# Kernel tuning notes

Hardware: AMD Instinct MI355X
Metric: run time of the kernel (lower is better)

The kernel has to match this reference:

```python
import jax, jax.numpy as jnp
import numpy as np

N_NODES = 50000
N_EDGES = 800000
NFEAT, NHID, NCLASS = 512, 128, 64


def setup_inputs() -> dict:
    key = jax.random.key(0)
    ks = jax.random.split(key, 8)
    x = jax.random.normal(ks[0], (N_NODES, NFEAT), dtype=jnp.float32)
    # GraphConvolution params (uniform-ish init like reset_parameters, stdv = 1/sqrt(fan_out))
    W1 = jax.random.normal(ks[1], (NFEAT, NHID), dtype=jnp.float32) * (1.0 / np.sqrt(NHID))
    b1 = jnp.zeros((NHID,), dtype=jnp.float32)
    W2 = jax.random.normal(ks[2], (NHID, NCLASS), dtype=jnp.float32) * (1.0 / np.sqrt(NCLASS))
    b2 = jnp.zeros((NCLASS,), dtype=jnp.float32)
    # sparse normalized adjacency in COO form
    edge_row = jax.random.randint(ks[3], (N_EDGES,), 0, N_NODES, dtype=jnp.int32)
    edge_col = jax.random.randint(ks[4], (N_EDGES,), 0, N_NODES, dtype=jnp.int32)
    edge_val = jax.random.uniform(ks[5], (N_EDGES,), dtype=jnp.float32) * 0.1
    return {"x": x, "W1": W1, "b1": b1, "W2": W2, "b2": b2,
            "edge_val": edge_val, "edge_row": edge_row, "edge_col": edge_col}


def _spmm(feat, edge_row, edge_col, edge_val, n_nodes):
    # (adj @ feat) with adj given as COO: out[r] = sum_e val[e] * feat[c[e]]
    msg = feat[edge_col] * edge_val[:, None]          # [E, d]
    return jax.ops.segment_sum(msg, edge_row, num_segments=n_nodes)


def reference(x, W1, b1, W2, b2, edge_val, edge_row, edge_col):
    # eval mode: dropout = identity, use_bn = False
    n = x.shape[0]
    h = jax.nn.relu(_spmm(x @ W1, edge_row, edge_col, edge_val, n) + b1)  # gc1 + relu
    out = _spmm(h @ W2, edge_row, edge_col, edge_val, n) + b2             # gc2
    return out
```

## Files before the change

### kernel.cpp

```cpp
#include <hip/hip_runtime.h>

#define N_NODES 50000
#define N_EDGES 800000
#define NFEAT 512
#define NHID 128
#define NCLASS 64

#define SCAN_BLOCKS 49
#define ZERO_BLOCKS 49

using bf16x8 = __attribute__((ext_vector_type(8))) __bf16;
using f32x4  = __attribute__((ext_vector_type(4))) float;
using u16x8  = __attribute__((ext_vector_type(8))) unsigned short;
using u16x4  = __attribute__((ext_vector_type(4))) unsigned short;
typedef unsigned long long u64;

__device__ __forceinline__ unsigned short f2bf(float f)
{
    unsigned u = __builtin_bit_cast(unsigned, f);
    unsigned r = (u + 0x7FFFu + ((u >> 16) & 1u)) >> 16;
    return (unsigned short)r;
}
__device__ __forceinline__ float bf2f(unsigned short b)
{
    return __builtin_bit_cast(float, (unsigned)b << 16);
}
__device__ __forceinline__ u16x4 cvt4(float4 f)
{
    u16x4 h;
    h[0] = __builtin_bit_cast(unsigned short, (__bf16)f.x);
    h[1] = __builtin_bit_cast(unsigned short, (__bf16)f.y);
    h[2] = __builtin_bit_cast(unsigned short, (__bf16)f.z);
    h[3] = __builtin_bit_cast(unsigned short, (__bf16)f.w);
    return h;
}

__global__ void prep_kernel(int4* __restrict__ zp, int n4,
                            const float* __restrict__ W1, const float* __restrict__ W2,
                            unsigned short* __restrict__ W1t, unsigned short* __restrict__ W2t)
{
    const int b = blockIdx.x;
    if (b < ZERO_BLOCKS) {
        const int i = b * 256 + threadIdx.x;
        if (i < n4) zp[i] = make_int4(0, 0, 0, 0);
    } else {
        const int idx = (b - ZERO_BLOCKS) * 256 + threadIdx.x;
        if (idx < NFEAT * NHID) {
            const int n = idx / NFEAT, k = idx % NFEAT;
            W1t[idx] = f2bf(W1[k * NHID + n]);
        } else {
            const int j = idx - NFEAT * NHID;
            if (j < NHID * NCLASS) {
                const int n = j / NHID, k = j % NHID;
                W2t[j] = f2bf(W2[k * NCLASS + n]);
            }
        }
    }
}

__global__ __launch_bounds__(512) void gemm1_pipe(const float* __restrict__ A,
                                                  const unsigned short* __restrict__ Bt,
                                                  unsigned short* __restrict__ C, int M)
{
    constexpr int K = NFEAT, N = NHID, BM = 128, BK = 32, NSTEP = K / BK;
    constexpr int LDW = BK + 8;
    __shared__ unsigned short As[2][BM][LDW];
    __shared__ unsigned short Bs[2][N][LDW];

    const int tid  = threadIdx.x;
    const int wid  = tid >> 6;
    const int lane = tid & 63;
    const int lm   = lane & 15;
    const int lk   = (lane >> 4) * 8;
    const int m0   = blockIdx.x * BM;

    const int ar0 = tid >> 3;
    const int ac0 = (tid & 7) * 4;
    const int ga0 = (m0 + ar0      < M) ? (m0 + ar0)      : (M - 1);
    const int ga1 = (m0 + ar0 + 64 < M) ? (m0 + ar0 + 64) : (M - 1);
    const float* Arow0 = &A[(size_t)ga0 * K];
    const float* Arow1 = &A[(size_t)ga1 * K];
    const int bn = tid >> 2;
    const int bk = (tid & 3) * 8;
    const unsigned short* Brow = &Bt[(size_t)bn * K];

    f32x4 acc[8] = {};

    {
        float4 fa0 = *(const float4*)&Arow0[ac0];
        float4 fa1 = *(const float4*)&Arow1[ac0];
        u16x8  bv  = *(const u16x8*)&Brow[bk];
        *(u16x4*)&As[0][ar0][ac0]      = cvt4(fa0);
        *(u16x4*)&As[0][ar0 + 64][ac0] = cvt4(fa1);
        *(u16x8*)&Bs[0][bn][bk]        = bv;
    }
    __syncthreads();

    #pragma unroll
    for (int t = 0; t < NSTEP; ++t) {
        const int cur = t & 1;
        float4 na0, na1; u16x8 nb;
        if (t + 1 < NSTEP) {
            na0 = *(const float4*)&Arow0[(t + 1) * BK + ac0];
            na1 = *(const float4*)&Arow1[(t + 1) * BK + ac0];
            nb  = *(const u16x8*)&Brow[(t + 1) * BK + bk];
        }
        bf16x8 a = __builtin_bit_cast(bf16x8, *(const u16x8*)&As[cur][wid * 16 + lm][lk]);
        #pragma unroll
        for (int nf = 0; nf < 8; ++nf) {
            bf16x8 b = __builtin_bit_cast(bf16x8, *(const u16x8*)&Bs[cur][nf * 16 + lm][lk]);
            acc[nf] = __builtin_amdgcn_mfma_f32_16x16x32_bf16(a, b, acc[nf], 0, 0, 0);
        }
        if (t + 1 < NSTEP) {
            *(u16x4*)&As[cur ^ 1][ar0][ac0]      = cvt4(na0);
            *(u16x4*)&As[cur ^ 1][ar0 + 64][ac0] = cvt4(na1);
            *(u16x8*)&Bs[cur ^ 1][bn][bk]        = nb;
            __syncthreads();
        }
    }

    #pragma unroll
    for (int nf = 0; nf < 8; ++nf)
        #pragma unroll
        for (int r = 0; r < 4; ++r) {
            const int m = m0 + wid * 16 + (lane >> 4) * 4 + r;
            if (m < M) C[(size_t)m * N + nf * 16 + lm] =
                __builtin_bit_cast(unsigned short, (__bf16)acc[nf][r]);
        }
}

template<int K, int N>
__global__ __launch_bounds__(256) void gemm_mfma_bf16a(const unsigned short* __restrict__ A,
                                                       const unsigned short* __restrict__ Bt,
                                                       unsigned short* __restrict__ C, int M)
{
    constexpr int BM = 128, BK = 32, NF = N / 16;
    constexpr int LDW = BK + 8;
    __shared__ unsigned short As[BM][LDW];
    __shared__ unsigned short Bs[N][LDW];

    const int tid  = threadIdx.x;
    const int wid  = tid >> 6;
    const int lane = tid & 63;
    const int lm   = lane & 15;
    const int lk   = (lane >> 4) * 8;
    const int m0   = blockIdx.x * BM;

    f32x4 acc[2][NF] = {};

    for (int k0 = 0; k0 < K; k0 += BK) {
        if (k0) __syncthreads();
        {
            #pragma unroll
            for (int c = 0; c < 2; ++c) {
                const int chunk = tid * 2 + c;
                const int r  = chunk >> 2;
                const int kc = (chunk & 3) * 8;
                const int m  = m0 + r;
                u16x8 v = {};
                if (m < M) v = *(const u16x8*)&A[(size_t)m * K + k0 + kc];
                *(u16x8*)&As[r][kc] = v;
            }
        }
        {
            constexpr int CH  = (N * BK / 8) / 256;
            constexpr int CPR = BK / 8;
            #pragma unroll
            for (int c = 0; c < CH; ++c) {
                const int chunk = tid * CH + c;
                const int n  = chunk / CPR;
                const int kc = (chunk % CPR) * 8;
                *(u16x8*)&Bs[n][kc] = *(const u16x8*)&Bt[(size_t)n * K + k0 + kc];
            }
        }
        __syncthreads();

        bf16x8 a[2];
        #pragma unroll
        for (int mf = 0; mf < 2; ++mf)
            a[mf] = __builtin_bit_cast(bf16x8, *(const u16x8*)&As[wid * 32 + mf * 16 + lm][lk]);
        #pragma unroll
        for (int nf = 0; nf < NF; ++nf) {
            bf16x8 b = __builtin_bit_cast(bf16x8, *(const u16x8*)&Bs[nf * 16 + lm][lk]);
            #pragma unroll
            for (int mf = 0; mf < 2; ++mf)
                acc[mf][nf] = __builtin_amdgcn_mfma_f32_16x16x32_bf16(a[mf], b, acc[mf][nf], 0, 0, 0);
        }
    }

    #pragma unroll
    for (int mf = 0; mf < 2; ++mf)
        #pragma unroll
        for (int nf = 0; nf < NF; ++nf)
            #pragma unroll
            for (int r = 0; r < 4; ++r) {
                const int m = m0 + wid * 32 + mf * 16 + (lane >> 4) * 4 + r;
                if (m < M) C[(size_t)m * N + nf * 16 + lm] =
                    __builtin_bit_cast(unsigned short, (__bf16)acc[mf][nf][r]);
            }
}

__global__ void hist_rank_kernel(const int* __restrict__ er, int* __restrict__ counts,
                                 unsigned char* __restrict__ rank)
{
    int e = blockIdx.x * blockDim.x + threadIdx.x;
    if (e < N_EDGES) rank[e] = (unsigned char)atomicAdd(&counts[er[e]], 1);
}

__global__ __launch_bounds__(1024) void scan_blocks(const int* __restrict__ counts,
                                                    int* __restrict__ row_ptr,
                                                    int* __restrict__ bsums)
{
    __shared__ int tmp[1024];
    const int tid = threadIdx.x;
    const int gid = blockIdx.x * 1024 + tid;
    const int v = (gid < N_NODES) ? counts[gid] : 0;
    tmp[tid] = v;
    __syncthreads();
    #pragma unroll
    for (int off = 1; off < 1024; off <<= 1) {
        int t = (tid >= off) ? tmp[tid - off] : 0;
        __syncthreads();
        tmp[tid] += t;
        __syncthreads();
    }
    if (gid < N_NODES) row_ptr[gid] = tmp[tid] - v;
    if (tid == 1023) bsums[blockIdx.x] = tmp[1023];
}

__global__ __launch_bounds__(1024) void add_offsets2(int* __restrict__ row_ptr,
                                                     const int* __restrict__ bsums)
{
    __shared__ int soff;
    if (threadIdx.x < 64) {
        const int lane = threadIdx.x;
        const int orig = (lane < SCAN_BLOCKS) ? bsums[lane] : 0;
        int v = orig;
        #pragma unroll
        for (int off = 1; off < 64; off <<= 1) {
            int t = __shfl_up(v, off, 64);
            if (lane >= off) v += t;
        }
        if (lane == (int)blockIdx.x) soff = v - orig;
    }
    __syncthreads();
    const int gid = blockIdx.x * 1024 + threadIdx.x;
    if (gid < N_NODES) row_ptr[gid] += soff;
    if (gid == 0) row_ptr[N_NODES] = N_EDGES;
}

__global__ void scatter_cv(const int* __restrict__ er, const int* __restrict__ ec,
                           const float* __restrict__ ev, const unsigned char* __restrict__ rank,
                           const int* __restrict__ row_ptr, unsigned* __restrict__ cv)
{
    int e = blockIdx.x * blockDim.x + threadIdx.x;
    if (e >= N_EDGES) return;
    const int r = er[e];
    const int pos = row_ptr[r] + (int)rank[e];
    cv[pos] = ((unsigned)f2bf(ev[e]) << 16) | (unsigned)ec[e];
}

__global__ __launch_bounds__(256) void spmm_bf16_h(const unsigned short* __restrict__ feat,
                                                   const int* __restrict__ row_ptr,
                                                   const unsigned* __restrict__ cv,
                                                   const float* __restrict__ bias,
                                                   unsigned short* __restrict__ out)
{
    const int wave = blockIdx.x * (blockDim.x >> 6) + (threadIdx.x >> 6);
    const int lane = threadIdx.x & 63;
    if (wave >= N_NODES) return;
    const int beg = row_ptr[wave];
    const int end = row_ptr[wave + 1];
    const int deg = end - beg;
    const int n1 = deg < 64 ? deg : 64;

    unsigned pcv = 0;
    if (lane < n1) pcv = cv[beg + lane];
    const int half = lane >> 5;
    const int qi   = (lane & 31) * 4;

    float ax[4][4] = {};
    for (int u = 0; u < n1; u += 8) {
        unsigned p[4];
        #pragma unroll
        for (int g = 0; g < 4; ++g) {
            const int idx = u + 2 * g + half;
            const int s = idx < n1 ? idx : 0;
            const unsigned t = __shfl(pcv, s, 64);
            p[g] = (idx < n1) ? t : 0u;
        }
        u16x4 w[4];
        #pragma unroll
        for (int g = 0; g < 4; ++g)
            w[g] = *(const u16x4*)&feat[(size_t)(p[g] & 0xFFFFu) * NHID + qi];
        #pragma unroll
        for (int g = 0; g < 4; ++g) {
            const float v = bf2f((unsigned short)(p[g] >> 16));
            #pragma unroll
            for (int j = 0; j < 4; ++j)
                ax[g][j] += v * bf2f(w[g][j]);
        }
    }
    for (int i = beg + 64 + half; i < end; i += 2) {
        const unsigned pp = cv[i];
        const float v = bf2f((unsigned short)(pp >> 16));
        const u16x4 w = *(const u16x4*)&feat[(size_t)(pp & 0xFFFFu) * NHID + qi];
        #pragma unroll
        for (int j = 0; j < 4; ++j) ax[0][j] += v * bf2f(w[j]);
    }

    float s[4];
    #pragma unroll
    for (int j = 0; j < 4; ++j) {
        s[j] = (ax[0][j] + ax[1][j]) + (ax[2][j] + ax[3][j]);
        s[j] += __shfl_xor(s[j], 32, 64);
    }
    if (half == 0) {
        const float4 bb = *(const float4*)&bias[qi];
        u16x4 o;
        o[0] = __builtin_bit_cast(unsigned short, (__bf16)fmaxf(s[0] + bb.x, 0.f));
        o[1] = __builtin_bit_cast(unsigned short, (__bf16)fmaxf(s[1] + bb.y, 0.f));
        o[2] = __builtin_bit_cast(unsigned short, (__bf16)fmaxf(s[2] + bb.z, 0.f));
        o[3] = __builtin_bit_cast(unsigned short, (__bf16)fmaxf(s[3] + bb.w, 0.f));
        *(u16x4*)&out[(size_t)wave * NHID + qi] = o;
    }
}

__global__ __launch_bounds__(256) void spmm_bf16_o(const unsigned short* __restrict__ feat,
                                                   const int* __restrict__ row_ptr,
                                                   const unsigned* __restrict__ cv,
                                                   const float* __restrict__ bias,
                                                   float* __restrict__ out)
{
    const int wave = blockIdx.x * (blockDim.x >> 6) + (threadIdx.x >> 6);
    const int lane = threadIdx.x & 63;
    if (wave >= N_NODES) return;
    const int beg = row_ptr[wave];
    const int end = row_ptr[wave + 1];
    const int deg = end - beg;
    const int n1 = deg < 64 ? deg : 64;

    unsigned pcv = 0;
    if (lane < n1) pcv = cv[beg + lane];
    const int grp = lane >> 4;
    const int qi  = (lane & 15) * 4;

    float a[2][4] = {};
    for (int u = 0; u < n1; u += 8) {
        unsigned p[2];
        #pragma unroll
        for (int g = 0; g < 2; ++g) {
            const int idx = u + 4 * g + grp;
            const int s = idx < n1 ? idx : 0;
            const unsigned t = __shfl(pcv, s, 64);
            p[g] = (idx < n1) ? t : 0u;
        }
        u16x4 w[2];
        #pragma unroll
        for (int g = 0; g < 2; ++g)
            w[g] = *(const u16x4*)&feat[(size_t)(p[g] & 0xFFFFu) * NCLASS + qi];
        #pragma unroll
        for (int g = 0; g < 2; ++g) {
            const float v = bf2f((unsigned short)(p[g] >> 16));
            #pragma unroll
            for (int j = 0; j < 4; ++j)
                a[g][j] += v * bf2f(w[g][j]);
        }
    }
    for (int i = beg + 64 + grp; i < end; i += 4) {
        const unsigned pp = cv[i];
        const float v = bf2f((unsigned short)(pp >> 16));
        const u16x4 w = *(const u16x4*)&feat[(size_t)(pp & 0xFFFFu) * NCLASS + qi];
        #pragma unroll
        for (int j = 0; j < 4; ++j) a[0][j] += v * bf2f(w[j]);
    }

    float s[4];
    #pragma unroll
    for (int j = 0; j < 4; ++j) {
        s[j] = a[0][j] + a[1][j];
        s[j] += __shfl_xor(s[j], 16, 64);
        s[j] += __shfl_xor(s[j], 32, 64);
    }
    if (lane < 16) {
        const float4 bb = *(const float4*)&bias[qi];
        float4 o = make_float4(s[0] + bb.x, s[1] + bb.y, s[2] + bb.z, s[3] + bb.w);
        *(float4*)&out[(size_t)wave * NCLASS + qi] = o;
    }
}

extern "C" void kernel_launch(void* const* d_in, const int* in_sizes, int n_in,
                              void* d_out, int out_size, void* d_ws, size_t ws_size,
                              hipStream_t stream)
{
    const float* x  = (const float*)d_in[0];
    const float* W1 = (const float*)d_in[1];
    const float* b1 = (const float*)d_in[2];
    const float* W2 = (const float*)d_in[3];
    const float* b2 = (const float*)d_in[4];
    const float* ev = (const float*)d_in[5];
    const int*   er = (const int*)d_in[6];
    const int*   ec = (const int*)d_in[7];
    float* out = (float*)d_out;

    unsigned* cv = (unsigned*)d_ws;
    unsigned char* rank = (unsigned char*)(cv + N_EDGES);
    unsigned short* XW1  = (unsigned short*)(rank + N_EDGES);
    unsigned short* Hpre = XW1 + (size_t)N_NODES * NHID;
    int* row_ptr = (int*)(Hpre + (size_t)N_NODES * NHID);
    int* counts  = row_ptr + 50016;
    int* bsums   = counts + 50016;
    unsigned short* W1t = (unsigned short*)(bsums + 64);
    unsigned short* W2t = W1t + NFEAT * NHID;

    unsigned short* HW2 = XW1;

    {
        const int n4 = (50016 + 64) / 4;
        const int conv_blocks = (NFEAT * NHID + NHID * NCLASS + 255) / 256;
        prep_kernel<<<ZERO_BLOCKS + conv_blocks, 256, 0, stream>>>(
            (int4*)counts, n4, W1, W2, W1t, W2t);
    }
    hist_rank_kernel<<<(N_EDGES + 255) / 256, 256, 0, stream>>>(er, counts, rank);
    scan_blocks<<<SCAN_BLOCKS, 1024, 0, stream>>>(counts, row_ptr, bsums);
    add_offsets2<<<SCAN_BLOCKS, 1024, 0, stream>>>(row_ptr, bsums);
    scatter_cv<<<(N_EDGES + 255) / 256, 256, 0, stream>>>(er, ec, ev, rank, row_ptr, cv);

    gemm1_pipe<<<(N_NODES + 127) / 128, 512, 0, stream>>>(x, W1t, XW1, N_NODES);
    spmm_bf16_h<<<(N_NODES + 3) / 4, 256, 0, stream>>>(XW1, row_ptr, cv, b1, Hpre);
    gemm_mfma_bf16a<NHID, NCLASS><<<(N_NODES + 127) / 128, 256, 0, stream>>>(Hpre, W2t, HW2, N_NODES);
    spmm_bf16_o<<<(N_NODES + 3) / 4, 256, 0, stream>>>(HW2, row_ptr, cv, b2, out);
}
```

Before: 148.7 us.

## Fuse scan phases into one kernel and merge edge scatter into GEMM1 launch

Replaces the two-kernel block scan (block scan plus offset add) with a single kernel in which each block recomputes its prefix by summing all earlier counts directly. It also folds the CSR scatter into the first GEMM launch as extra blocks, so the scatter work runs alongside the GEMM tiles. This removes two kernel launches and their serialization gaps. In exchange, later scan blocks redundantly read up to about 50K counts each, and the scatter blocks carry the GEMM's shared-memory footprint and 512-thread size, which may limit occupancy.

```diff
diff --git a/kernel.cpp b/kernel.cpp
--- a/kernel.cpp
+++ b/kernel.cpp
@@ -8,12 +8,13 @@
 
 #define SCAN_BLOCKS 49
 #define ZERO_BLOCKS 49
+#define GB1 391
+#define SCAT_BLOCKS 1563
 
 using bf16x8 = __attribute__((ext_vector_type(8))) __bf16;
 using f32x4  = __attribute__((ext_vector_type(4))) float;
 using u16x8  = __attribute__((ext_vector_type(8))) unsigned short;
 using u16x4  = __attribute__((ext_vector_type(4))) unsigned short;
-typedef unsigned long long u64;
 
 __device__ __forceinline__ unsigned short f2bf(float f)
 {
@@ -58,14 +59,67 @@
     }
 }
 
-__global__ __launch_bounds__(512) void gemm1_pipe(const float* __restrict__ A,
-                                                  const unsigned short* __restrict__ Bt,
-                                                  unsigned short* __restrict__ C, int M)
+__global__ void hist_rank_kernel(const int* __restrict__ er, int* __restrict__ counts,
+                                 unsigned char* __restrict__ rank)
+{
+    int e = blockIdx.x * blockDim.x + threadIdx.x;
+    if (e < N_EDGES) rank[e] = (unsigned char)atomicAdd(&counts[er[e]], 1);
+}
+
+__global__ __launch_bounds__(1024) void scan_fused(const int* __restrict__ counts,
+                                                   int* __restrict__ row_ptr)
+{
+    __shared__ int tmp[1024];
+    __shared__ int bpre;
+    const int tid = threadIdx.x;
+    const int b = blockIdx.x;
+    const int gid = b * 1024 + tid;
+    int pre = 0;
+    for (int i = tid; i < b * 1024; i += 1024) pre += counts[i];
+    tmp[tid] = pre;
+    __syncthreads();
+    #pragma unroll
+    for (int off = 512; off > 0; off >>= 1) {
+        if (tid < off) tmp[tid] += tmp[tid + off];
+        __syncthreads();
+    }
+    if (tid == 0) bpre = tmp[0];
+    __syncthreads();
+    const int v = (gid < N_NODES) ? counts[gid] : 0;
+    tmp[tid] = v;
+    __syncthreads();
+    #pragma unroll
+    for (int off = 1; off < 1024; off <<= 1) {
+        int t = (tid >= off) ? tmp[tid - off] : 0;
+        __syncthreads();
+        tmp[tid] += t;
+        __syncthreads();
+    }
+    if (gid < N_NODES) row_ptr[gid] = bpre + tmp[tid] - v;
+    if (gid == 0) row_ptr[N_NODES] = N_EDGES;
+}
+
+__global__ __launch_bounds__(512) void gemm1_scatter(
+    const float* __restrict__ A, const unsigned short* __restrict__ Bt,
+    unsigned short* __restrict__ C, int M,
+    const int* __restrict__ er, const int* __restrict__ ec,
+    const float* __restrict__ ev, const unsigned char* __restrict__ rank,
+    const int* __restrict__ row_ptr, unsigned* __restrict__ cv)
 {
     constexpr int K = NFEAT, N = NHID, BM = 128, BK = 32, NSTEP = K / BK;
     constexpr int LDW = BK + 8;
     __shared__ unsigned short As[2][BM][LDW];
     __shared__ unsigned short Bs[2][N][LDW];
+
+    if (blockIdx.x >= GB1) {
+        const int e = (blockIdx.x - GB1) * 512 + threadIdx.x;
+        if (e < N_EDGES) {
+            const int r = er[e];
+            const int pos = row_ptr[r] + (int)rank[e];
+            cv[pos] = ((unsigned)f2bf(ev[e]) << 16) | (unsigned)ec[e];
+        }
+        return;
+    }
 
     const int tid  = threadIdx.x;
     const int wid  = tid >> 6;
@@ -200,66 +254,6 @@
             }
 }
 
-__global__ void hist_rank_kernel(const int* __restrict__ er, int* __restrict__ counts,
-                                 unsigned char* __restrict__ rank)
-{
-    int e = blockIdx.x * blockDim.x + threadIdx.x;
-    if (e < N_EDGES) rank[e] = (unsigned char)atomicAdd(&counts[er[e]], 1);
-}
-
-__global__ __launch_bounds__(1024) void scan_blocks(const int* __restrict__ counts,
-                                                    int* __restrict__ row_ptr,
-                                                    int* __restrict__ bsums)
-{
-    __shared__ int tmp[1024];
-    const int tid = threadIdx.x;
-    const int gid = blockIdx.x * 1024 + tid;
-    const int v = (gid < N_NODES) ? counts[gid] : 0;
-    tmp[tid] = v;
-    __syncthreads();
-    #pragma unroll
-    for (int off = 1; off < 1024; off <<= 1) {
-        int t = (tid >= off) ? tmp[tid - off] : 0;
-        __syncthreads();
-        tmp[tid] += t;
-        __syncthreads();
-    }
-    if (gid < N_NODES) row_ptr[gid] = tmp[tid] - v;
-    if (tid == 1023) bsums[blockIdx.x] = tmp[1023];
-}
-
-__global__ __launch_bounds__(1024) void add_offsets2(int* __restrict__ row_ptr,
-                                                     const int* __restrict__ bsums)
-{
-    __shared__ int soff;
-    if (threadIdx.x < 64) {
-        const int lane = threadIdx.x;
-        const int orig = (lane < SCAN_BLOCKS) ? bsums[lane] : 0;
-        int v = orig;
-        #pragma unroll
-        for (int off = 1; off < 64; off <<= 1) {
-            int t = __shfl_up(v, off, 64);
-            if (lane >= off) v += t;
-        }
-        if (lane == (int)blockIdx.x) soff = v - orig;
-    }
-    __syncthreads();
-    const int gid = blockIdx.x * 1024 + threadIdx.x;
-    if (gid < N_NODES) row_ptr[gid] += soff;
-    if (gid == 0) row_ptr[N_NODES] = N_EDGES;
-}
-
-__global__ void scatter_cv(const int* __restrict__ er, const int* __restrict__ ec,
-                           const float* __restrict__ ev, const unsigned char* __restrict__ rank,
-                           const int* __restrict__ row_ptr, unsigned* __restrict__ cv)
-{
-    int e = blockIdx.x * blockDim.x + threadIdx.x;
-    if (e >= N_EDGES) return;
-    const int r = er[e];
-    const int pos = row_ptr[r] + (int)rank[e];
-    cv[pos] = ((unsigned)f2bf(ev[e]) << 16) | (unsigned)ec[e];
-}
-
 __global__ __launch_bounds__(256) void spmm_bf16_h(const unsigned short* __restrict__ feat,
                                                    const int* __restrict__ row_ptr,
                                                    const unsigned* __restrict__ cv,
@@ -409,24 +403,23 @@
     unsigned short* Hpre = XW1 + (size_t)N_NODES * NHID;
     int* row_ptr = (int*)(Hpre + (size_t)N_NODES * NHID);
     int* counts  = row_ptr + 50016;
-    int* bsums   = counts + 50016;
-    unsigned short* W1t = (unsigned short*)(bsums + 64);
+    unsigned short* W1t = (unsigned short*)(counts + 50016);
     unsigned short* W2t = W1t + NFEAT * NHID;
 
     unsigned short* HW2 = XW1;
 
     {
-        const int n4 = (50016 + 64) / 4;
+        const int n4 = 50016 / 4;
         const int conv_blocks = (NFEAT * NHID + NHID * NCLASS + 255) / 256;
         prep_kernel<<<ZERO_BLOCKS + conv_blocks, 256, 0, stream>>>(
             (int4*)counts, n4, W1, W2, W1t, W2t);
     }
     hist_rank_kernel<<<(N_EDGES + 255) / 256, 256, 0, stream>>>(er, counts, rank);
-    scan_blocks<<<SCAN_BLOCKS, 1024, 0, stream>>>(counts, row_ptr, bsums);
-    add_offsets2<<<SCAN_BLOCKS, 1024, 0, stream>>>(row_ptr, bsums);
-    scatter_cv<<<(N_EDGES + 255) / 256, 256, 0, stream>>>(er, ec, ev, rank, row_ptr, cv);
-
-    gemm1_pipe<<<(N_NODES + 127) / 128, 512, 0, stream>>>(x, W1t, XW1, N_NODES);
+    scan_fused<<<SCAN_BLOCKS, 1024, 0, stream>>>(counts, row_ptr);
+
+    gemm1_scatter<<<GB1 + SCAT_BLOCKS, 512, 0, stream>>>(
+        x, W1t, XW1, N_NODES, er, ec, ev, rank, row_ptr, cv);
+
     spmm_bf16_h<<<(N_NODES + 3) / 4, 256, 0, stream>>>(XW1, row_ptr, cv, b1, Hpre);
     gemm_mfma_bf16a<NHID, NCLASS><<<(N_NODES + 127) / 128, 256, 0, stream>>>(Hpre, W2t, HW2, N_NODES);
     spmm_bf16_o<<<(N_NODES + 3) / 4, 256, 0, stream>>>(HW2, row_ptr, cv, b2, out);
```

After: 149.9 us. About the same (+0.8%).
